# Kernel optimization log

Hardware: AMD Instinct MI355X
Metric: run time of the kernel (lower is better)

Reference implementation:

```python
import jax, jax.numpy as jnp
import numpy as np

B, L, D = 16, 512, 512
H, DK, DV = 8, 64, 64
TEMP = float(np.sqrt(DK))  # temperature = d_k ** 0.5
FC_IN = L * H * DK         # 262144, dynamic fc created in forward (combination==0)
FC_OUT = H * DK            # 512


def setup_inputs() -> dict:
    key = jax.random.key(0)
    ks = jax.random.split(key, 11)
    s_qk = np.sqrt(2.0 / (D + DK)).astype(np.float32)
    s_v = np.sqrt(2.0 / (D + DV)).astype(np.float32)
    return {
        "q": jax.random.normal(ks[0], (B, L, D), jnp.float32),
        "k": jax.random.normal(ks[1], (B, L, D), jnp.float32),
        "v": jax.random.normal(ks[2], (B, L, D), jnp.float32),
        "Wq": jax.random.normal(ks[3], (H * DK, D), jnp.float32) * s_qk,
        "bq": jnp.zeros((H * DK,), jnp.float32),
        "Wk": jax.random.normal(ks[4], (H * DK, D), jnp.float32) * s_qk,
        "bk": jnp.zeros((H * DK,), jnp.float32),
        "Wv": jax.random.normal(ks[5], (H * DV, D), jnp.float32) * s_v,
        "bv": jnp.zeros((H * DV,), jnp.float32),
        # fc created dynamically in forward: Linear(L*H*DK, H*DK)
        "Wf": jax.random.normal(ks[6], (FC_OUT, FC_IN), jnp.float32) * (1.0 / np.sqrt(FC_IN)),
        "bf": jnp.zeros((FC_OUT,), jnp.float32),
    }


def reference(q, k, v, Wq, bq, Wk, bk, Wv, bv, Wf, bf):
    # projections -> [B, L, H, d]
    qh = (q @ Wq.T + bq).reshape(B, L, H, DK)
    kh = (k @ Wk.T + bk).reshape(B, L, H, DK)
    vh = (v @ Wv.T + bv).reshape(B, L, H, DV)
    # scores [H, B, Lq, Lk] (matches permute(2,0,1,3).view(-1,L,dk) head-major order)
    scores = jnp.einsum('bqhd,bkhd->hbqk', qh, kh) / TEMP
    attn = jax.nn.softmax(scores, axis=-1)  # softmax over keys; dropout is identity in eval
    out = jnp.einsum('hbqk,bkhd->bqhd', attn, vh)  # [B, Lq, H, DV]
    out_flat = out.reshape(B, L * H * DV)          # [B, L*H*DV]
    output = out_flat @ Wf.T + bf                  # dynamic fc, dropout identity
    attn_flat = attn.reshape(H * B, L, L)
    return (output, attn_flat)
```

## Files before the change

### kernel.cpp

```cpp
#include <hip/hip_runtime.h>
#include <hip/hip_bf16.h>

typedef __attribute__((ext_vector_type(4))) float f32x4;
typedef __attribute__((ext_vector_type(8))) short s16x8;
typedef __attribute__((ext_vector_type(4))) unsigned short u16x4;


__device__ __forceinline__ unsigned short f2bf(float f) {
    unsigned int u = __builtin_bit_cast(unsigned int, f);
    u += 0x7fffu + ((u >> 16) & 1u);
    return (unsigned short)(u >> 16);
}

__global__ __launch_bounds__(256) void proj_kernel(
    const float* __restrict__ q, const float* __restrict__ k, const float* __restrict__ v,
    const float* __restrict__ Wq, const float* __restrict__ bq,
    const float* __restrict__ Wk, const float* __restrict__ bk,
    const float* __restrict__ Wv, const float* __restrict__ bv,
    unsigned short* __restrict__ qh, unsigned short* __restrict__ kh, unsigned short* __restrict__ vh)
{
    const int z = blockIdx.z;
    const float* X    = (z == 0) ? q  : (z == 1) ? k  : v;
    const float* W    = (z == 0) ? Wq : (z == 1) ? Wk : Wv;
    const float* bias = (z == 0) ? bq : (z == 1) ? bk : bv;
    unsigned short* out = (z == 0) ? qh : (z == 1) ? kh : vh;

    __shared__ __align__(16) unsigned short lA[128 * 40];
    __shared__ __align__(16) unsigned short lB[128 * 40];

    const int t = threadIdx.x;
    const int m0 = blockIdx.x * 128;
    const int n0 = blockIdx.y * 128;
    const int wave = t >> 6, lane = t & 63, quad = lane >> 4, l16 = lane & 15;
    const int wm = (wave >> 1) * 64, wn = (wave & 1) * 64;

    f32x4 acc[4][4];
#pragma unroll
    for (int i = 0; i < 4; i++)
#pragma unroll
        for (int j = 0; j < 4; j++) acc[i][j] = (f32x4){0.f, 0.f, 0.f, 0.f};

    for (int k0 = 0; k0 < 512; k0 += 32) {
#pragma unroll
        for (int it = 0; it < 4; it++) {
            int idx = it * 256 + t;
            int row = idx >> 3, c = (idx & 7) * 4;
            f32x4 xa = *(const f32x4*)(X + (size_t)(m0 + row) * 512 + k0 + c);
            u16x4 pa = {f2bf(xa.x), f2bf(xa.y), f2bf(xa.z), f2bf(xa.w)};
            *(u16x4*)&lA[row * 40 + c] = pa;
            f32x4 xb = *(const f32x4*)(W + (size_t)(n0 + row) * 512 + k0 + c);
            u16x4 pb = {f2bf(xb.x), f2bf(xb.y), f2bf(xb.z), f2bf(xb.w)};
            *(u16x4*)&lB[row * 40 + c] = pb;
        }
        __syncthreads();
        s16x8 af[4], bm[4];
#pragma unroll
        for (int i = 0; i < 4; i++) af[i] = *(const s16x8*)&lA[(wm + i * 16 + l16) * 40 + quad * 8];
#pragma unroll
        for (int j = 0; j < 4; j++) bm[j] = *(const s16x8*)&lB[(wn + j * 16 + l16) * 40 + quad * 8];
#pragma unroll
        for (int i = 0; i < 4; i++)
#pragma unroll
            for (int j = 0; j < 4; j++)
                acc[i][j] = __builtin_amdgcn_mfma_f32_16x16x32_bf16(af[i], bm[j], acc[i][j], 0, 0, 0);
        __syncthreads();
    }
#pragma unroll
    for (int j = 0; j < 4; j++) {
        int n = n0 + wn + j * 16 + l16;
        float bb = bias[n];
        int h = n >> 6, d = n & 63;
#pragma unroll
        for (int i = 0; i < 4; i++) {
#pragma unroll
            for (int r = 0; r < 4; r++) {
                int m = m0 + wm + i * 16 + quad * 4 + r;
                int b = m >> 9, l = m & 511;
                out[(size_t)((b * 8 + h) * 512 + l) * 64 + d] = f2bf(acc[i][j][r] + bb);
            }
        }
    }
}

__global__ __launch_bounds__(256) void transpose_v(const unsigned short* __restrict__ vh,
                                                   unsigned short* __restrict__ vhT)
{
    __shared__ unsigned short lT[64 * 72];
    const int bh = blockIdx.x;
    const int k0 = blockIdx.y * 64;
    const int t = threadIdx.x;
    const unsigned short* src = vh + (size_t)bh * 32768;
    unsigned short* dst = vhT + (size_t)bh * 32768;
#pragma unroll
    for (int it = 0; it < 4; it++) {
        int idx = it * 256 + t;
        int row = idx >> 4, c = (idx & 15) * 4;
        *(u16x4*)&lT[row * 72 + c] = *(const u16x4*)(src + (size_t)(k0 + row) * 64 + c);
    }
    __syncthreads();
#pragma unroll
    for (int it = 0; it < 16; it++) {
        int idx = it * 256 + t;
        int d = idx >> 6, kk = idx & 63;
        dst[(size_t)d * 512 + k0 + kk] = lT[kk * 72 + d];
    }
}

__global__ void init_out(float* __restrict__ out, const float* __restrict__ bf)
{
    int i = blockIdx.x * 256 + threadIdx.x;
    if (i < 8192) out[i] = bf[i & 511];
}

__global__ __launch_bounds__(256) void attn_kernel(
    const unsigned short* __restrict__ qh, const unsigned short* __restrict__ kh,
    const unsigned short* __restrict__ vhT,
    float* __restrict__ dout, unsigned short* __restrict__ ofl)
{
    __shared__ __align__(16) unsigned short lp[4][16][520];
    const int bh = blockIdx.y;
    const int h = bh >> 4, b = bh & 15;
    const int q0 = blockIdx.x * 64;
    const int t = threadIdx.x;
    const int w = t >> 6, lane = t & 63, quad = lane >> 4, l16 = lane & 15;
    const size_t base = (size_t)(b * 8 + h) * 32768;
    const unsigned short* qb = qh + base;
    const unsigned short* kb = kh + base;
    const unsigned short* vb = vhT + base;

    const int qrow = q0 + w * 16 + l16;
    s16x8 aq0 = *(const s16x8*)(qb + (size_t)qrow * 64 + quad * 8);
    s16x8 aq1 = *(const s16x8*)(qb + (size_t)qrow * 64 + 32 + quad * 8);

    f32x4 acc[32];
#pragma unroll
    for (int tt = 0; tt < 32; tt++) acc[tt] = (f32x4){0.f, 0.f, 0.f, 0.f};

#pragma unroll
    for (int tt = 0; tt < 32; tt++) {
        const unsigned short* kp = kb + (size_t)(tt * 16 + l16) * 64 + quad * 8;
        s16x8 b0 = *(const s16x8*)kp;
        s16x8 b1 = *(const s16x8*)(kp + 32);
        acc[tt] = __builtin_amdgcn_mfma_f32_16x16x32_bf16(aq0, b0, acc[tt], 0, 0, 0);
        acc[tt] = __builtin_amdgcn_mfma_f32_16x16x32_bf16(aq1, b1, acc[tt], 0, 0, 0);
    }

    float mx[4] = {-1e30f, -1e30f, -1e30f, -1e30f};
#pragma unroll
    for (int tt = 0; tt < 32; tt++)
#pragma unroll
        for (int r = 0; r < 4; r++) {
            float s = acc[tt][r] * 0.125f;
            acc[tt][r] = s;
            mx[r] = fmaxf(mx[r], s);
        }
#pragma unroll
    for (int r = 0; r < 4; r++) {
        float m = mx[r];
        m = fmaxf(m, __shfl_xor(m, 1));
        m = fmaxf(m, __shfl_xor(m, 2));
        m = fmaxf(m, __shfl_xor(m, 4));
        m = fmaxf(m, __shfl_xor(m, 8));
        mx[r] = m;
    }
    float sm[4] = {0.f, 0.f, 0.f, 0.f};
#pragma unroll
    for (int tt = 0; tt < 32; tt++)
#pragma unroll
        for (int r = 0; r < 4; r++) {
            float e = __expf(acc[tt][r] - mx[r]);
            acc[tt][r] = e;
            sm[r] += e;
        }
    float inv[4];
#pragma unroll
    for (int r = 0; r < 4; r++) {
        float s = sm[r];
        s += __shfl_xor(s, 1);
        s += __shfl_xor(s, 2);
        s += __shfl_xor(s, 4);
        s += __shfl_xor(s, 8);
        inv[r] = 1.0f / s;
    }

    float* attn_out = dout + 8192;
#pragma unroll
    for (int r = 0; r < 4; r++) {
        int qq = q0 + w * 16 + quad * 4 + r;
        float* rp = attn_out + (size_t)bh * 262144 + (size_t)qq * 512 + l16;
        float iv = inv[r];
#pragma unroll
        for (int tt = 0; tt < 32; tt++) {
            float p = acc[tt][r] * iv;
            rp[tt * 16] = p;
            lp[w][quad * 4 + r][tt * 16 + l16] = f2bf(p);
        }
    }

    f32x4 oacc[4];
#pragma unroll
    for (int j = 0; j < 4; j++) oacc[j] = (f32x4){0.f, 0.f, 0.f, 0.f};
#pragma unroll
    for (int ks = 0; ks < 16; ks++) {
        s16x8 pa = *(const s16x8*)&lp[w][l16][ks * 32 + quad * 8];
#pragma unroll
        for (int j = 0; j < 4; j++) {
            s16x8 bv = *(const s16x8*)(vb + (size_t)(j * 16 + l16) * 512 + ks * 32 + quad * 8);
            oacc[j] = __builtin_amdgcn_mfma_f32_16x16x32_bf16(pa, bv, oacc[j], 0, 0, 0);
        }
    }
#pragma unroll
    for (int j = 0; j < 4; j++) {
#pragma unroll
        for (int r = 0; r < 4; r++) {
            int qq = q0 + w * 16 + quad * 4 + r;
            int d = j * 16 + l16;
            ofl[(size_t)b * 262144 + (size_t)(qq * 8 + h) * 64 + d] = f2bf(oacc[j][r]);
        }
    }
}

__global__ __launch_bounds__(512) void fc_kernel(
    const unsigned short* __restrict__ ofl, const float* __restrict__ Wf,
    float* __restrict__ out)
{
    __shared__ __align__(16) float red[8][4][64][4];
    const int t = threadIdx.x;
    const int w = t >> 6, lane = t & 63, quad = lane >> 4, l16 = lane & 15;
    const int n0 = blockIdx.x * 64;
    const int kbase = blockIdx.y * 4096 + w * 512;

    f32x4 acc[4];
#pragma unroll
    for (int j = 0; j < 4; j++) acc[j] = (f32x4){0.f, 0.f, 0.f, 0.f};

#pragma unroll
    for (int ks = 0; ks < 16; ks++) {
        int kk = kbase + ks * 32;
        s16x8 af = *(const s16x8*)(ofl + (size_t)l16 * 262144 + kk + quad * 8);
#pragma unroll
        for (int j = 0; j < 4; j++) {
            const float* wp = Wf + (size_t)(n0 + j * 16 + l16) * 262144 + kk + quad * 8;
            f32x4 w0 = *(const f32x4*)wp;
            f32x4 w1 = *(const f32x4*)(wp + 4);
            s16x8 bv = {(short)f2bf(w0.x), (short)f2bf(w0.y), (short)f2bf(w0.z), (short)f2bf(w0.w),
                        (short)f2bf(w1.x), (short)f2bf(w1.y), (short)f2bf(w1.z), (short)f2bf(w1.w)};
            acc[j] = __builtin_amdgcn_mfma_f32_16x16x32_bf16(af, bv, acc[j], 0, 0, 0);
        }
    }
#pragma unroll
    for (int j = 0; j < 4; j++) *(f32x4*)&red[w][j][lane][0] = acc[j];
    __syncthreads();
    if (t < 256) {
        int j = t >> 6, ln = t & 63;
        f32x4 s = (f32x4){0.f, 0.f, 0.f, 0.f};
#pragma unroll
        for (int wv = 0; wv < 8; wv++) s += *(const f32x4*)&red[wv][j][ln][0];
        int qd = ln >> 4, lo = ln & 15;
        int o = n0 + j * 16 + lo;
#pragma unroll
        for (int r = 0; r < 4; r++) atomicAdd(&out[(qd * 4 + r) * 512 + o], s[r]);
    }
}

extern "C" void kernel_launch(void* const* d_in, const int* in_sizes, int n_in,
                              void* d_out, int out_size, void* d_ws, size_t ws_size,
                              hipStream_t stream)
{
    const float* q  = (const float*)d_in[0];
    const float* k  = (const float*)d_in[1];
    const float* v  = (const float*)d_in[2];
    const float* Wq = (const float*)d_in[3];
    const float* bq = (const float*)d_in[4];
    const float* Wk = (const float*)d_in[5];
    const float* bk = (const float*)d_in[6];
    const float* Wv = (const float*)d_in[7];
    const float* bv = (const float*)d_in[8];
    const float* Wf = (const float*)d_in[9];
    const float* bf = (const float*)d_in[10];

    unsigned short* qh  = (unsigned short*)d_ws;
    unsigned short* kh  = qh  + 4194304;
    unsigned short* vh  = kh  + 4194304;
    unsigned short* vhT = vh  + 4194304;
    unsigned short* ofl = vhT + 4194304;
    float* out = (float*)d_out;

    hipLaunchKernelGGL(proj_kernel, dim3(64, 4, 3), dim3(256), 0, stream,
                       q, k, v, Wq, bq, Wk, bk, Wv, bv, qh, kh, vh);
    hipLaunchKernelGGL(transpose_v, dim3(128, 8), dim3(256), 0, stream, vh, vhT);
    hipLaunchKernelGGL(init_out, dim3(32), dim3(256), 0, stream, out, bf);
    hipLaunchKernelGGL(attn_kernel, dim3(8, 128), dim3(256), 0, stream, qh, kh, vhT, out, ofl);
    hipLaunchKernelGGL(fc_kernel, dim3(8, 64), dim3(512), 0, stream, ofl, Wf, out);
}
```

Measured before the change: 881.0 us.

## Fuse V transpose into projection, transpose QK^T for vectorized softmax and stores

The V projection now writes its output directly in transposed [d, l] layout with packed stores, which removes the separate transpose kernel and its extra global round trip. The attention score MFMA swaps operands so each lane holds four consecutive keys for one query row. That allows cross-lane max and sum reductions with only two shuffles, exp2 with a prescaled constant, and 16-byte nontemporal stores of the attention matrix. Other changes add packed bf16 conversion in the projection loads, nontemporal loads of Wf in the fc kernel, and s_setprio around the MFMA loops. Gains are expected from cutting a kernel launch and from wider memory transactions, at the cost of strided 8-byte writes in the V epilogue.

```diff
diff --git a/kernel.cpp b/kernel.cpp
--- a/kernel.cpp
+++ b/kernel.cpp
@@ -1,15 +1,22 @@
 #include <hip/hip_runtime.h>
 #include <hip/hip_bf16.h>
+#include <math.h>
 
 typedef __attribute__((ext_vector_type(4))) float f32x4;
 typedef __attribute__((ext_vector_type(8))) short s16x8;
 typedef __attribute__((ext_vector_type(4))) unsigned short u16x4;
+typedef __attribute__((ext_vector_type(2))) unsigned int u32x2;
+typedef __attribute__((ext_vector_type(4))) unsigned int u32x4;
 
 
 __device__ __forceinline__ unsigned short f2bf(float f) {
     unsigned int u = __builtin_bit_cast(unsigned int, f);
     u += 0x7fffu + ((u >> 16) & 1u);
     return (unsigned short)(u >> 16);
+}
+
+__device__ __forceinline__ unsigned int cvtpk(float lo, float hi) {
+    return (unsigned int)f2bf(lo) | ((unsigned int)f2bf(hi) << 16);
 }
 
 __global__ __launch_bounds__(256) void proj_kernel(
@@ -17,13 +24,13 @@
     const float* __restrict__ Wq, const float* __restrict__ bq,
     const float* __restrict__ Wk, const float* __restrict__ bk,
     const float* __restrict__ Wv, const float* __restrict__ bv,
-    unsigned short* __restrict__ qh, unsigned short* __restrict__ kh, unsigned short* __restrict__ vh)
+    unsigned short* __restrict__ qh, unsigned short* __restrict__ kh, unsigned short* __restrict__ vhT)
 {
     const int z = blockIdx.z;
     const float* X    = (z == 0) ? q  : (z == 1) ? k  : v;
     const float* W    = (z == 0) ? Wq : (z == 1) ? Wk : Wv;
     const float* bias = (z == 0) ? bq : (z == 1) ? bk : bv;
-    unsigned short* out = (z == 0) ? qh : (z == 1) ? kh : vh;
+    unsigned short* out = (z == 0) ? qh : (z == 1) ? kh : vhT;
 
     __shared__ __align__(16) unsigned short lA[128 * 40];
     __shared__ __align__(16) unsigned short lB[128 * 40];
@@ -46,11 +53,11 @@
             int idx = it * 256 + t;
             int row = idx >> 3, c = (idx & 7) * 4;
             f32x4 xa = *(const f32x4*)(X + (size_t)(m0 + row) * 512 + k0 + c);
-            u16x4 pa = {f2bf(xa.x), f2bf(xa.y), f2bf(xa.z), f2bf(xa.w)};
-            *(u16x4*)&lA[row * 40 + c] = pa;
+            u32x2 pa = { cvtpk(xa.x, xa.y), cvtpk(xa.z, xa.w) };
+            *(u32x2*)&lA[row * 40 + c] = pa;
             f32x4 xb = *(const f32x4*)(W + (size_t)(n0 + row) * 512 + k0 + c);
-            u16x4 pb = {f2bf(xb.x), f2bf(xb.y), f2bf(xb.z), f2bf(xb.w)};
-            *(u16x4*)&lB[row * 40 + c] = pb;
+            u32x2 pb = { cvtpk(xb.x, xb.y), cvtpk(xb.z, xb.w) };
+            *(u32x2*)&lB[row * 40 + c] = pb;
         }
         __syncthreads();
         s16x8 af[4], bm[4];
@@ -65,44 +72,37 @@
                 acc[i][j] = __builtin_amdgcn_mfma_f32_16x16x32_bf16(af[i], bm[j], acc[i][j], 0, 0, 0);
         __syncthreads();
     }
-#pragma unroll
-    for (int j = 0; j < 4; j++) {
-        int n = n0 + wn + j * 16 + l16;
-        float bb = bias[n];
-        int h = n >> 6, d = n & 63;
-#pragma unroll
-        for (int i = 0; i < 4; i++) {
-#pragma unroll
-            for (int r = 0; r < 4; r++) {
-                int m = m0 + wm + i * 16 + quad * 4 + r;
+    if (z == 2) {
+#pragma unroll
+        for (int j = 0; j < 4; j++) {
+            int n = n0 + wn + j * 16 + l16;
+            float bb = bias[n];
+            int h = n >> 6, d = n & 63;
+#pragma unroll
+            for (int i = 0; i < 4; i++) {
+                int m = m0 + wm + i * 16 + quad * 4;
                 int b = m >> 9, l = m & 511;
-                out[(size_t)((b * 8 + h) * 512 + l) * 64 + d] = f2bf(acc[i][j][r] + bb);
+                u32x2 pk2 = { cvtpk(acc[i][j][0] + bb, acc[i][j][1] + bb),
+                              cvtpk(acc[i][j][2] + bb, acc[i][j][3] + bb) };
+                *(u32x2*)(out + (size_t)((b * 8 + h) * 64 + d) * 512 + l) = pk2;
             }
         }
-    }
-}
-
-__global__ __launch_bounds__(256) void transpose_v(const unsigned short* __restrict__ vh,
-                                                   unsigned short* __restrict__ vhT)
-{
-    __shared__ unsigned short lT[64 * 72];
-    const int bh = blockIdx.x;
-    const int k0 = blockIdx.y * 64;
-    const int t = threadIdx.x;
-    const unsigned short* src = vh + (size_t)bh * 32768;
-    unsigned short* dst = vhT + (size_t)bh * 32768;
-#pragma unroll
-    for (int it = 0; it < 4; it++) {
-        int idx = it * 256 + t;
-        int row = idx >> 4, c = (idx & 15) * 4;
-        *(u16x4*)&lT[row * 72 + c] = *(const u16x4*)(src + (size_t)(k0 + row) * 64 + c);
-    }
-    __syncthreads();
-#pragma unroll
-    for (int it = 0; it < 16; it++) {
-        int idx = it * 256 + t;
-        int d = idx >> 6, kk = idx & 63;
-        dst[(size_t)d * 512 + k0 + kk] = lT[kk * 72 + d];
+    } else {
+#pragma unroll
+        for (int j = 0; j < 4; j++) {
+            int n = n0 + wn + j * 16 + l16;
+            float bb = bias[n];
+            int h = n >> 6, d = n & 63;
+#pragma unroll
+            for (int i = 0; i < 4; i++) {
+#pragma unroll
+                for (int r = 0; r < 4; r++) {
+                    int m = m0 + wm + i * 16 + quad * 4 + r;
+                    int b = m >> 9, l = m & 511;
+                    out[(size_t)((b * 8 + h) * 512 + l) * 64 + d] = f2bf(acc[i][j][r] + bb);
+                }
+            }
+        }
     }
 }
 
@@ -129,86 +129,74 @@
     const unsigned short* vb = vhT + base;
 
     const int qrow = q0 + w * 16 + l16;
-    s16x8 aq0 = *(const s16x8*)(qb + (size_t)qrow * 64 + quad * 8);
-    s16x8 aq1 = *(const s16x8*)(qb + (size_t)qrow * 64 + 32 + quad * 8);
+    s16x8 bq0 = *(const s16x8*)(qb + (size_t)qrow * 64 + quad * 8);
+    s16x8 bq1 = *(const s16x8*)(qb + (size_t)qrow * 64 + 32 + quad * 8);
 
     f32x4 acc[32];
 #pragma unroll
     for (int tt = 0; tt < 32; tt++) acc[tt] = (f32x4){0.f, 0.f, 0.f, 0.f};
 
+    __builtin_amdgcn_s_setprio(1);
 #pragma unroll
     for (int tt = 0; tt < 32; tt++) {
         const unsigned short* kp = kb + (size_t)(tt * 16 + l16) * 64 + quad * 8;
-        s16x8 b0 = *(const s16x8*)kp;
-        s16x8 b1 = *(const s16x8*)(kp + 32);
-        acc[tt] = __builtin_amdgcn_mfma_f32_16x16x32_bf16(aq0, b0, acc[tt], 0, 0, 0);
-        acc[tt] = __builtin_amdgcn_mfma_f32_16x16x32_bf16(aq1, b1, acc[tt], 0, 0, 0);
-    }
-
-    float mx[4] = {-1e30f, -1e30f, -1e30f, -1e30f};
+        s16x8 a0 = *(const s16x8*)kp;
+        s16x8 a1 = *(const s16x8*)(kp + 32);
+        acc[tt] = __builtin_amdgcn_mfma_f32_16x16x32_bf16(a0, bq0, acc[tt], 0, 0, 0);
+        acc[tt] = __builtin_amdgcn_mfma_f32_16x16x32_bf16(a1, bq1, acc[tt], 0, 0, 0);
+    }
+    __builtin_amdgcn_s_setprio(0);
+
+    const float C1 = 0.18033688011112042f;
+    float mx = -1e30f;
 #pragma unroll
     for (int tt = 0; tt < 32; tt++)
 #pragma unroll
         for (int r = 0; r < 4; r++) {
-            float s = acc[tt][r] * 0.125f;
+            float s = acc[tt][r] * C1;
             acc[tt][r] = s;
-            mx[r] = fmaxf(mx[r], s);
-        }
-#pragma unroll
-    for (int r = 0; r < 4; r++) {
-        float m = mx[r];
-        m = fmaxf(m, __shfl_xor(m, 1));
-        m = fmaxf(m, __shfl_xor(m, 2));
-        m = fmaxf(m, __shfl_xor(m, 4));
-        m = fmaxf(m, __shfl_xor(m, 8));
-        mx[r] = m;
-    }
-    float sm[4] = {0.f, 0.f, 0.f, 0.f};
+            mx = fmaxf(mx, s);
+        }
+    mx = fmaxf(mx, __shfl_xor(mx, 16));
+    mx = fmaxf(mx, __shfl_xor(mx, 32));
+    float sum = 0.f;
 #pragma unroll
     for (int tt = 0; tt < 32; tt++)
 #pragma unroll
         for (int r = 0; r < 4; r++) {
-            float e = __expf(acc[tt][r] - mx[r]);
+            float e = exp2f(acc[tt][r] - mx);
             acc[tt][r] = e;
-            sm[r] += e;
-        }
-    float inv[4];
-#pragma unroll
-    for (int r = 0; r < 4; r++) {
-        float s = sm[r];
-        s += __shfl_xor(s, 1);
-        s += __shfl_xor(s, 2);
-        s += __shfl_xor(s, 4);
-        s += __shfl_xor(s, 8);
-        inv[r] = 1.0f / s;
-    }
-
-    float* attn_out = dout + 8192;
-#pragma unroll
-    for (int r = 0; r < 4; r++) {
-        int qq = q0 + w * 16 + quad * 4 + r;
-        float* rp = attn_out + (size_t)bh * 262144 + (size_t)qq * 512 + l16;
-        float iv = inv[r];
-#pragma unroll
-        for (int tt = 0; tt < 32; tt++) {
-            float p = acc[tt][r] * iv;
-            rp[tt * 16] = p;
-            lp[w][quad * 4 + r][tt * 16 + l16] = f2bf(p);
-        }
+            sum += e;
+        }
+    sum += __shfl_xor(sum, 16);
+    sum += __shfl_xor(sum, 32);
+    const float inv = 1.0f / sum;
+
+    float* rp = dout + 8192 + (size_t)bh * 262144 + (size_t)qrow * 512 + quad * 4;
+#pragma unroll
+    for (int tt = 0; tt < 32; tt++) {
+        f32x4 p;
+#pragma unroll
+        for (int r = 0; r < 4; r++) p[r] = acc[tt][r] * inv;
+        __builtin_nontemporal_store(p, (f32x4*)(rp + tt * 16));
+        u32x2 pb = { cvtpk(p.x, p.y), cvtpk(p.z, p.w) };
+        *(u32x2*)&lp[w][l16][tt * 16 + quad * 4] = pb;
     }
 
     f32x4 oacc[4];
 #pragma unroll
     for (int j = 0; j < 4; j++) oacc[j] = (f32x4){0.f, 0.f, 0.f, 0.f};
+    __builtin_amdgcn_s_setprio(1);
 #pragma unroll
     for (int ks = 0; ks < 16; ks++) {
         s16x8 pa = *(const s16x8*)&lp[w][l16][ks * 32 + quad * 8];
 #pragma unroll
         for (int j = 0; j < 4; j++) {
-            s16x8 bv = *(const s16x8*)(vb + (size_t)(j * 16 + l16) * 512 + ks * 32 + quad * 8);
-            oacc[j] = __builtin_amdgcn_mfma_f32_16x16x32_bf16(pa, bv, oacc[j], 0, 0, 0);
-        }
-    }
+            s16x8 bvv = *(const s16x8*)(vb + (size_t)(j * 16 + l16) * 512 + ks * 32 + quad * 8);
+            oacc[j] = __builtin_amdgcn_mfma_f32_16x16x32_bf16(pa, bvv, oacc[j], 0, 0, 0);
+        }
+    }
+    __builtin_amdgcn_s_setprio(0);
 #pragma unroll
     for (int j = 0; j < 4; j++) {
 #pragma unroll
@@ -241,11 +229,12 @@
 #pragma unroll
         for (int j = 0; j < 4; j++) {
             const float* wp = Wf + (size_t)(n0 + j * 16 + l16) * 262144 + kk + quad * 8;
-            f32x4 w0 = *(const f32x4*)wp;
-            f32x4 w1 = *(const f32x4*)(wp + 4);
-            s16x8 bv = {(short)f2bf(w0.x), (short)f2bf(w0.y), (short)f2bf(w0.z), (short)f2bf(w0.w),
-                        (short)f2bf(w1.x), (short)f2bf(w1.y), (short)f2bf(w1.z), (short)f2bf(w1.w)};
-            acc[j] = __builtin_amdgcn_mfma_f32_16x16x32_bf16(af, bv, acc[j], 0, 0, 0);
+            f32x4 w0 = __builtin_nontemporal_load((const f32x4*)wp);
+            f32x4 w1 = __builtin_nontemporal_load((const f32x4*)wp + 1);
+            u32x4 pw = { cvtpk(w0.x, w0.y), cvtpk(w0.z, w0.w),
+                         cvtpk(w1.x, w1.y), cvtpk(w1.z, w1.w) };
+            s16x8 bvv = __builtin_bit_cast(s16x8, pw);
+            acc[j] = __builtin_amdgcn_mfma_f32_16x16x32_bf16(af, bvv, acc[j], 0, 0, 0);
         }
     }
 #pragma unroll
@@ -281,14 +270,12 @@
 
     unsigned short* qh  = (unsigned short*)d_ws;
     unsigned short* kh  = qh  + 4194304;
-    unsigned short* vh  = kh  + 4194304;
-    unsigned short* vhT = vh  + 4194304;
+    unsigned short* vhT = kh  + 4194304;
     unsigned short* ofl = vhT + 4194304;
     float* out = (float*)d_out;
 
     hipLaunchKernelGGL(proj_kernel, dim3(64, 4, 3), dim3(256), 0, stream,
-                       q, k, v, Wq, bq, Wk, bk, Wv, bv, qh, kh, vh);
-    hipLaunchKernelGGL(transpose_v, dim3(128, 8), dim3(256), 0, stream, vh, vhT);
+                       q, k, v, Wq, bq, Wk, bk, Wv, bv, qh, kh, vhT);
     hipLaunchKernelGGL(init_out, dim3(32), dim3(256), 0, stream, out, bf);
     hipLaunchKernelGGL(attn_kernel, dim3(8, 128), dim3(256), 0, stream, qh, kh, vhT, out, ofl);
     hipLaunchKernelGGL(fc_kernel, dim3(8, 64), dim3(512), 0, stream, ofl, Wf, out);
```

Measured after the change: 904.6 us. 1.03x slower.
